# Performance work log

Measured on AMD Instinct MI355X. Metric: run time of the kernel, lower is better.

## Reference

```python
import jax, jax.numpy as jnp
import numpy as np

NUM_CLASSES = 10
BASE_TEMPERATURE = 0.07
TEMP = 0.1


def setup_inputs() -> dict:
    key = jax.random.key(0)
    k1, k2 = jax.random.split(key)
    features = jax.random.normal(k1, (8192, 128), dtype=jnp.float32)
    targets = jax.random.randint(k2, (8192,), 0, NUM_CLASSES, dtype=jnp.int64)
    return {"features": features, "targets": targets}


def reference(features, targets):
    bs = features.shape[0]
    dtype = features.dtype
    # one-hot label matrix -> positive mask via label agreement
    one_hot = jax.nn.one_hot(targets, NUM_CLASSES, dtype=dtype)          # [bs, C]
    mask_pos_full = one_hot @ one_hot.T                                  # [bs, bs], 1 if same class
    mask_negatives = jnp.ones((bs, bs), dtype=dtype) - mask_pos_full
    mask_positives = mask_pos_full - jnp.eye(bs, dtype=dtype)            # exclude self
    logits_mask = mask_positives + mask_negatives                        # == 1 - eye
    # pairwise similarity logits
    logits = (features @ features.T) / TEMP                              # [bs, bs]
    logits_max = jax.lax.stop_gradient(jnp.max(logits, axis=1, keepdims=True))
    logits = logits - logits_max
    exp_logits = jnp.exp(logits) * logits_mask
    log_prob = logits - jnp.log(jnp.sum(exp_logits, axis=1, keepdims=True) + 1e-20)
    mean_log_prob_pos = jnp.sum(mask_positives * log_prob, axis=1) / (
        jnp.sum(mask_positives, axis=1) + 1e-20
    )
    loss = -(TEMP / BASE_TEMPERATURE) * jnp.mean(mean_log_prob_pos)
    avg_pos = jnp.mean(jnp.sum(mask_positives, axis=1))
    avg_neg = jnp.mean(jnp.sum(mask_negatives, axis=1))
    return (loss, avg_pos, avg_neg)
```

## Files before the change

### kernel.cpp

```cpp
#include <hip/hip_runtime.h>

#define N 8192
#define KD 128
#define NCLS 10
#define NCH 8
#define CHUNK (N / NCH)

typedef __attribute__((ext_vector_type(4))) float floatx4;


__global__ __launch_bounds__(256) void k_conv(const float* __restrict__ F,
                                              const int* __restrict__ tgt,
                                              float* __restrict__ diag10,
                                              int* __restrict__ A10,
                                              int* __restrict__ B1,
                                              float* __restrict__ S,
                                              int* __restrict__ cnt,
                                              float* __restrict__ PS) {
    int t = threadIdx.x;
    if (blockIdx.x < 512) {
        int row0 = blockIdx.x * 16;
        if (t < 16) PS[row0 + t] = 0.f;
        int col4 = t & 31;
        int rg = t >> 5;
#pragma unroll
        for (int sw = 0; sw < 2; ++sw) {
            int row = row0 + sw * 8 + rg;
            float4 v = *(const float4*)(F + (size_t)row * KD + col4 * 4);
            float sq = v.x * v.x + v.y * v.y + v.z * v.z + v.w * v.w;
#pragma unroll
            for (int off = 16; off >= 1; off >>= 1) sq += __shfl_xor(sq, off);
            if (col4 == 0) diag10[row] = 10.f * sq;
            int da = __builtin_amdgcn_cvt_pk_fp8_f32(10.f * v.x, 10.f * v.y, 0, false);
            da = __builtin_amdgcn_cvt_pk_fp8_f32(10.f * v.z, 10.f * v.w, da, true);
            int db = __builtin_amdgcn_cvt_pk_fp8_f32(v.x, v.y, 0, false);
            db = __builtin_amdgcn_cvt_pk_fp8_f32(v.z, v.w, db, true);
            int rt = row >> 4, rl = row & 15;
            int ks = col4 >> 3, quad = (col4 & 7) >> 1, half = col4 & 1;
            int idx = rt * 512 + ks * 128 + quad * 32 + rl * 2 + half;
            A10[idx] = da;
            B1[idx] = db;
        }
    } else {
        int b = blockIdx.x - 512;
        int row0 = b * 128;
        int k = t & 127, h = t >> 7;
        __shared__ int lh[NCLS];
        if (t < NCLS) lh[t] = 0;
        __syncthreads();
        if (t < 128) atomicAdd(&lh[tgt[row0 + t]], 1);
        float local[NCLS];
#pragma unroll
        for (int c = 0; c < NCLS; ++c) local[c] = 0.f;
        for (int ii = 0; ii < 64; ++ii) {
            int row = row0 + h * 64 + ii;
            float v = F[(size_t)row * KD + k];
            int c = tgt[row];
#pragma unroll
            for (int cc = 0; cc < NCLS; ++cc) local[cc] += (cc == c) ? v : 0.f;
        }
        __shared__ float red[2][NCLS][KD];
#pragma unroll
        for (int cc = 0; cc < NCLS; ++cc) red[h][cc][k] = local[cc];
        __syncthreads();
        if (h == 0) {
#pragma unroll
            for (int cc = 0; cc < NCLS; ++cc)
                atomicAdd(&S[cc * KD + k], red[0][cc][k] + red[1][cc][k]);
            if (t < NCLS) atomicAdd(&cnt[t], lh[t]);
        }
    }
}

__global__ __launch_bounds__(256, 3) void k_pair(const unsigned char* __restrict__ Af,
                                                 const unsigned char* __restrict__ Bf,
                                                 const float* __restrict__ diag10,
                                                 float* __restrict__ PS) {
    int bx = blockIdx.x, ch = blockIdx.y;
    int tid = threadIdx.x;
    int w = tid >> 6, lane = tid & 63;
    int quad = lane >> 4, l16 = lane & 15;
    int row0 = bx * 64;

    float d = diag10[row0 + lane];
#pragma unroll
    for (int off = 32; off >= 1; off >>= 1) d = fminf(d, __shfl_xor(d, off));
    float thr = d - 60.f;

    long af[4][4];
#pragma unroll
    for (int it = 0; it < 4; ++it)
#pragma unroll
        for (int ks = 0; ks < 4; ++ks)
            af[it][ks] = *(const long*)(Af + (size_t)(bx * 4 + it) * 2048 + ks * 512 + lane * 8);

#pragma unroll
    for (int jj = 0; jj < 4; ++jj) {
        int col0 = ch * CHUNK + (jj * 4 + w) * 64;
        const unsigned char* bp = Bf + (size_t)(col0 >> 4) * 2048 + lane * 8;

        long bfr[4][4];
#pragma unroll
        for (int tj = 0; tj < 4; ++tj)
#pragma unroll
            for (int ks = 0; ks < 4; ++ks)
                bfr[tj][ks] = *(const long*)(bp + tj * 2048 + ks * 512);

        floatx4 acc[4][4];
#pragma unroll
        for (int it = 0; it < 4; ++it)
#pragma unroll
            for (int tj = 0; tj < 4; ++tj)
                acc[it][tj] = (floatx4){0.f, 0.f, 0.f, 0.f};

#pragma unroll
        for (int ks = 0; ks < 4; ++ks)
#pragma unroll
            for (int it = 0; it < 4; ++it)
#pragma unroll
                for (int tj = 0; tj < 4; ++tj)
                    acc[it][tj] = __builtin_amdgcn_mfma_f32_16x16x32_fp8_fp8(
                        af[it][ks], bfr[tj][ks], acc[it][tj], 0, 0, 0);

        float mx = -1e30f;
#pragma unroll
        for (int it = 0; it < 4; ++it)
#pragma unroll
            for (int tj = 0; tj < 4; ++tj) {
                float a01 = fmaxf(acc[it][tj][0], acc[it][tj][1]);
                float a23 = fmaxf(acc[it][tj][2], acc[it][tj][3]);
                mx = fmaxf(mx, fmaxf(a01, a23));
            }

        if (__any(mx > thr)) {
#pragma unroll
            for (int it = 0; it < 4; ++it)
#pragma unroll
                for (int r = 0; r < 4; ++r) {
                    int grow = row0 + it * 16 + quad * 4 + r;
                    float Mrow = diag10[grow];
                    float rs = 0.f;
#pragma unroll
                    for (int tj = 0; tj < 4; ++tj) {
                        int gcol = col0 + tj * 16 + l16;
                        float ev = __expf(acc[it][tj][r] - Mrow);
                        rs += (grow == gcol) ? 0.f : ev;
                    }
                    rs += __shfl_xor(rs, 1, 16);
                    rs += __shfl_xor(rs, 2, 16);
                    rs += __shfl_xor(rs, 4, 16);
                    rs += __shfl_xor(rs, 8, 16);
                    if (l16 == 0) atomicAdd(&PS[grow], rs);
                }
        }
    }
}

__global__ __launch_bounds__(256) void k_final(const float* __restrict__ F,
                                               const int* __restrict__ tgt,
                                               const float* __restrict__ diag10,
                                               const float* __restrict__ PS,
                                               const float* __restrict__ S,
                                               int* __restrict__ cnt,
                                               float* __restrict__ acc,
                                               float* __restrict__ out) {
    __shared__ float Ss[NCLS * KD];
    __shared__ int cs[NCLS];
    int t = threadIdx.x;
    for (int i = t; i < NCLS * KD; i += 256) Ss[i] = S[i];
    if (t < NCLS) cs[t] = cnt[t];
    __syncthreads();

    int g = t >> 2, q = t & 3;
    int row = blockIdx.x * 64 + g;
    int c = tgt[row];
    float dot = 0.f;
#pragma unroll
    for (int i = 0; i < 8; ++i) {
        float4 f = *(const float4*)(F + (size_t)row * KD + i * 16 + q * 4);
        float4 s = *(const float4*)(Ss + c * KD + i * 16 + q * 4);
        dot += f.x * s.x + f.y * s.y + f.z * s.z + f.w * s.w;
    }
    dot += __shfl_xor(dot, 1, 4);
    dot += __shfl_xor(dot, 2, 4);

    float mlp = 0.f;
    if (q == 0) {
        float M = diag10[row];
        float pp = 10.f * dot - M;
        float T = PS[row];
        float np = (float)(cs[c] - 1);
        mlp = (np < 0.5f) ? 0.f : (pp - np * (M + __logf(T + 1e-20f))) / np;
    }
#pragma unroll
    for (int off = 32; off >= 1; off >>= 1) mlp += __shfl_xor(mlp, off);
    __shared__ float wsum[4];
    int lane = t & 63, w = t >> 6;
    if (lane == 0) wsum[w] = mlp;
    __syncthreads();
    if (t == 0) {
        atomicAdd(acc, (wsum[0] + wsum[1]) + (wsum[2] + wsum[3]));
        __threadfence();
        int old = atomicAdd(&cnt[12], 1);
        if (old == (int)gridDim.x - 1) {
            float tot = atomicAdd(acc, 0.0f);
            double sp = 0.0, sn = 0.0;
            for (int cc = 0; cc < NCLS; ++cc) {
                double n = (double)cs[cc];
                sp += n * (n - 1.0);
                sn += n * ((double)N - n);
            }
            out[0] = (float)(-(0.1 / 0.07) * ((double)tot / (double)N));
            out[1] = (float)(sp / (double)N);
            out[2] = (float)(sn / (double)N);
        }
    }
}

extern "C" void kernel_launch(void* const* d_in, const int* in_sizes, int n_in,
                              void* d_out, int out_size, void* d_ws, size_t ws_size,
                              hipStream_t stream) {
    const float* F = (const float*)d_in[0];
    const int* tgt = (const int*)d_in[1];
    float* out = (float*)d_out;
    char* ws = (char*)d_ws;

    int* cnt = (int*)(ws);
    float* acc = (float*)(ws + 64);
    float* S = (float*)(ws + 128);
    float* PS = (float*)(ws + 8192);
    float* diag10 = (float*)(ws + 65536);
    int* A10 = (int*)(ws + (1u << 20));
    int* B1 = (int*)(ws + (2u << 20));

    hipMemsetAsync(ws, 0, 8192, stream);
    k_conv<<<576, 256, 0, stream>>>(F, tgt, diag10, A10, B1, S, cnt, PS);
    k_pair<<<dim3(N / 64, NCH), 256, 0, stream>>>((const unsigned char*)A10,
                                                  (const unsigned char*)B1, diag10, PS);
    k_final<<<N / 64, 256, 0, stream>>>(F, tgt, diag10, PS, S, cnt, acc, out);
}
```

Before: 98.07 us.

## Fuse class-sum reduction into conversion blocks and double pair-kernel column chunks

Each of the 512 conversion blocks now accumulates per-class feature sums and the label histogram in shared memory with LDS atomics, then flushes nonzero entries to global with atomics. This removes the separate 64 reduction blocks that each reread 128 rows. The pair kernel's column split goes from 8 to 16 chunks with half the inner iterations per block, giving more blocks for occupancy in exchange for reloading the A fragments more often. Global atomic traffic on S rises, since every block can touch up to 1280 entries.

```diff
diff --git a/kernel.cpp b/kernel.cpp
--- a/kernel.cpp
+++ b/kernel.cpp
@@ -3,7 +3,7 @@
 #define N 8192
 #define KD 128
 #define NCLS 10
-#define NCH 8
+#define NCH 16
 #define CHUNK (N / NCH)
 
 typedef __attribute__((ext_vector_type(4))) float floatx4;
@@ -17,59 +17,49 @@
                                               float* __restrict__ S,
                                               int* __restrict__ cnt,
                                               float* __restrict__ PS) {
+    __shared__ float red[NCLS][KD];
+    __shared__ int hist[NCLS];
     int t = threadIdx.x;
-    if (blockIdx.x < 512) {
-        int row0 = blockIdx.x * 16;
-        if (t < 16) PS[row0 + t] = 0.f;
-        int col4 = t & 31;
-        int rg = t >> 5;
-#pragma unroll
-        for (int sw = 0; sw < 2; ++sw) {
-            int row = row0 + sw * 8 + rg;
-            float4 v = *(const float4*)(F + (size_t)row * KD + col4 * 4);
-            float sq = v.x * v.x + v.y * v.y + v.z * v.z + v.w * v.w;
-#pragma unroll
-            for (int off = 16; off >= 1; off >>= 1) sq += __shfl_xor(sq, off);
-            if (col4 == 0) diag10[row] = 10.f * sq;
-            int da = __builtin_amdgcn_cvt_pk_fp8_f32(10.f * v.x, 10.f * v.y, 0, false);
-            da = __builtin_amdgcn_cvt_pk_fp8_f32(10.f * v.z, 10.f * v.w, da, true);
-            int db = __builtin_amdgcn_cvt_pk_fp8_f32(v.x, v.y, 0, false);
-            db = __builtin_amdgcn_cvt_pk_fp8_f32(v.z, v.w, db, true);
-            int rt = row >> 4, rl = row & 15;
-            int ks = col4 >> 3, quad = (col4 & 7) >> 1, half = col4 & 1;
-            int idx = rt * 512 + ks * 128 + quad * 32 + rl * 2 + half;
-            A10[idx] = da;
-            B1[idx] = db;
-        }
-    } else {
-        int b = blockIdx.x - 512;
-        int row0 = b * 128;
-        int k = t & 127, h = t >> 7;
-        __shared__ int lh[NCLS];
-        if (t < NCLS) lh[t] = 0;
-        __syncthreads();
-        if (t < 128) atomicAdd(&lh[tgt[row0 + t]], 1);
-        float local[NCLS];
-#pragma unroll
-        for (int c = 0; c < NCLS; ++c) local[c] = 0.f;
-        for (int ii = 0; ii < 64; ++ii) {
-            int row = row0 + h * 64 + ii;
-            float v = F[(size_t)row * KD + k];
-            int c = tgt[row];
-#pragma unroll
-            for (int cc = 0; cc < NCLS; ++cc) local[cc] += (cc == c) ? v : 0.f;
-        }
-        __shared__ float red[2][NCLS][KD];
-#pragma unroll
-        for (int cc = 0; cc < NCLS; ++cc) red[h][cc][k] = local[cc];
-        __syncthreads();
-        if (h == 0) {
-#pragma unroll
-            for (int cc = 0; cc < NCLS; ++cc)
-                atomicAdd(&S[cc * KD + k], red[0][cc][k] + red[1][cc][k]);
-            if (t < NCLS) atomicAdd(&cnt[t], lh[t]);
-        }
-    }
+    int row0 = blockIdx.x * 16;
+    if (t < NCLS) hist[t] = 0;
+    for (int i = t; i < NCLS * KD; i += 256) ((float*)red)[i] = 0.f;
+    __syncthreads();
+    if (t < 16) {
+        atomicAdd(&hist[tgt[row0 + t]], 1);
+        PS[row0 + t] = 0.f;
+    }
+
+    int col4 = t & 31;
+    int rg = t >> 5;
+#pragma unroll
+    for (int sw = 0; sw < 2; ++sw) {
+        int row = row0 + sw * 8 + rg;
+        float4 v = *(const float4*)(F + (size_t)row * KD + col4 * 4);
+        float sq = v.x * v.x + v.y * v.y + v.z * v.z + v.w * v.w;
+#pragma unroll
+        for (int off = 16; off >= 1; off >>= 1) sq += __shfl_xor(sq, off);
+        if (col4 == 0) diag10[row] = 10.f * sq;
+        int da = __builtin_amdgcn_cvt_pk_fp8_f32(10.f * v.x, 10.f * v.y, 0, false);
+        da = __builtin_amdgcn_cvt_pk_fp8_f32(10.f * v.z, 10.f * v.w, da, true);
+        int db = __builtin_amdgcn_cvt_pk_fp8_f32(v.x, v.y, 0, false);
+        db = __builtin_amdgcn_cvt_pk_fp8_f32(v.z, v.w, db, true);
+        int rt = row >> 4, rl = row & 15;
+        int ks = col4 >> 3, quad = (col4 & 7) >> 1, half = col4 & 1;
+        int idx = rt * 512 + ks * 128 + quad * 32 + rl * 2 + half;
+        A10[idx] = da;
+        B1[idx] = db;
+        int c = tgt[row];
+        atomicAdd(&red[c][col4 * 4 + 0], v.x);
+        atomicAdd(&red[c][col4 * 4 + 1], v.y);
+        atomicAdd(&red[c][col4 * 4 + 2], v.z);
+        atomicAdd(&red[c][col4 * 4 + 3], v.w);
+    }
+    __syncthreads();
+    for (int i = t; i < NCLS * KD; i += 256) {
+        float v = ((const float*)red)[i];
+        if (v != 0.f) atomicAdd(&S[i], v);
+    }
+    if (t < NCLS) atomicAdd(&cnt[t], hist[t]);
 }
 
 __global__ __launch_bounds__(256, 3) void k_pair(const unsigned char* __restrict__ Af,
@@ -95,7 +85,7 @@
             af[it][ks] = *(const long*)(Af + (size_t)(bx * 4 + it) * 2048 + ks * 512 + lane * 8);
 
 #pragma unroll
-    for (int jj = 0; jj < 4; ++jj) {
+    for (int jj = 0; jj < 2; ++jj) {
         int col0 = ch * CHUNK + (jj * 4 + w) * 64;
         const unsigned char* bp = Bf + (size_t)(col0 >> 4) * 2048 + lane * 8;
 
@@ -234,7 +224,7 @@
     int* B1 = (int*)(ws + (2u << 20));
 
     hipMemsetAsync(ws, 0, 8192, stream);
-    k_conv<<<576, 256, 0, stream>>>(F, tgt, diag10, A10, B1, S, cnt, PS);
+    k_conv<<<N / 16, 256, 0, stream>>>(F, tgt, diag10, A10, B1, S, cnt, PS);
     k_pair<<<dim3(N / 64, NCH), 256, 0, stream>>>((const unsigned char*)A10,
                                                   (const unsigned char*)B1, diag10, PS);
     k_final<<<N / 64, 256, 0, stream>>>(F, tgt, diag10, PS, S, cnt, acc, out);
```

Result: slower. 103.4 us (+5.5%).

## Fuse final reduction into pair kernel via per-row-block completion tickets

Applied to the files above, without the earlier changes.

Removes the separate k_final launch by having the last of the NCH chunk blocks for each row block (found with an atomic ticket counter per row block) compute that row block's loss contribution and the global finalization. This targets the launch gap and tail of an extra kernel. In exchange every pair block now pays a threadfence and an atomic, PS is read through an atomic to see other blocks' writes, and S and the class counts are read straight from global memory instead of being staged in LDS. The workspace layout is shifted so the tickets sit in the zeroed region.

```diff
diff --git a/kernel.cpp b/kernel.cpp
--- a/kernel.cpp
+++ b/kernel.cpp
@@ -75,7 +75,14 @@
 __global__ __launch_bounds__(256, 3) void k_pair(const unsigned char* __restrict__ Af,
                                                  const unsigned char* __restrict__ Bf,
                                                  const float* __restrict__ diag10,
-                                                 float* __restrict__ PS) {
+                                                 float* __restrict__ PS,
+                                                 const float* __restrict__ F,
+                                                 const int* __restrict__ tgt,
+                                                 const float* __restrict__ S,
+                                                 int* __restrict__ cnt,
+                                                 int* __restrict__ tk,
+                                                 float* __restrict__ acc,
+                                                 float* __restrict__ out) {
     int bx = blockIdx.x, ch = blockIdx.y;
     int tid = threadIdx.x;
     int w = tid >> 6, lane = tid & 63;
@@ -106,12 +113,12 @@
             for (int ks = 0; ks < 4; ++ks)
                 bfr[tj][ks] = *(const long*)(bp + tj * 2048 + ks * 512);
 
-        floatx4 acc[4][4];
+        floatx4 acm[4][4];
 #pragma unroll
         for (int it = 0; it < 4; ++it)
 #pragma unroll
             for (int tj = 0; tj < 4; ++tj)
-                acc[it][tj] = (floatx4){0.f, 0.f, 0.f, 0.f};
+                acm[it][tj] = (floatx4){0.f, 0.f, 0.f, 0.f};
 
 #pragma unroll
         for (int ks = 0; ks < 4; ++ks)
@@ -119,16 +126,16 @@
             for (int it = 0; it < 4; ++it)
 #pragma unroll
                 for (int tj = 0; tj < 4; ++tj)
-                    acc[it][tj] = __builtin_amdgcn_mfma_f32_16x16x32_fp8_fp8(
-                        af[it][ks], bfr[tj][ks], acc[it][tj], 0, 0, 0);
+                    acm[it][tj] = __builtin_amdgcn_mfma_f32_16x16x32_fp8_fp8(
+                        af[it][ks], bfr[tj][ks], acm[it][tj], 0, 0, 0);
 
         float mx = -1e30f;
 #pragma unroll
         for (int it = 0; it < 4; ++it)
 #pragma unroll
             for (int tj = 0; tj < 4; ++tj) {
-                float a01 = fmaxf(acc[it][tj][0], acc[it][tj][1]);
-                float a23 = fmaxf(acc[it][tj][2], acc[it][tj][3]);
+                float a01 = fmaxf(acm[it][tj][0], acm[it][tj][1]);
+                float a23 = fmaxf(acm[it][tj][2], acm[it][tj][3]);
                 mx = fmaxf(mx, fmaxf(a01, a23));
             }
 
@@ -143,7 +150,7 @@
 #pragma unroll
                     for (int tj = 0; tj < 4; ++tj) {
                         int gcol = col0 + tj * 16 + l16;
-                        float ev = __expf(acc[it][tj][r] - Mrow);
+                        float ev = __expf(acm[it][tj][r] - Mrow);
                         rs += (grow == gcol) ? 0.f : ev;
                     }
                     rs += __shfl_xor(rs, 1, 16);
@@ -154,31 +161,22 @@
                 }
         }
     }
-}
-
-__global__ __launch_bounds__(256) void k_final(const float* __restrict__ F,
-                                               const int* __restrict__ tgt,
-                                               const float* __restrict__ diag10,
-                                               const float* __restrict__ PS,
-                                               const float* __restrict__ S,
-                                               int* __restrict__ cnt,
-                                               float* __restrict__ acc,
-                                               float* __restrict__ out) {
-    __shared__ float Ss[NCLS * KD];
-    __shared__ int cs[NCLS];
-    int t = threadIdx.x;
-    for (int i = t; i < NCLS * KD; i += 256) Ss[i] = S[i];
-    if (t < NCLS) cs[t] = cnt[t];
+
+    __shared__ int winner;
+    __threadfence();
+    if (tid == 0) winner = (atomicAdd(&tk[bx], 1) == NCH - 1) ? 1 : 0;
     __syncthreads();
-
-    int g = t >> 2, q = t & 3;
-    int row = blockIdx.x * 64 + g;
+    if (!winner) return;
+    __threadfence();
+
+    int g = tid >> 2, q = tid & 3;
+    int row = row0 + g;
     int c = tgt[row];
     float dot = 0.f;
 #pragma unroll
     for (int i = 0; i < 8; ++i) {
         float4 f = *(const float4*)(F + (size_t)row * KD + i * 16 + q * 4);
-        float4 s = *(const float4*)(Ss + c * KD + i * 16 + q * 4);
+        float4 s = *(const float4*)(S + c * KD + i * 16 + q * 4);
         dot += f.x * s.x + f.y * s.y + f.z * s.z + f.w * s.w;
     }
     dot += __shfl_xor(dot, 1, 4);
@@ -188,25 +186,24 @@
     if (q == 0) {
         float M = diag10[row];
         float pp = 10.f * dot - M;
-        float T = PS[row];
-        float np = (float)(cs[c] - 1);
+        float T = atomicAdd(&PS[row], 0.f);
+        float np = (float)(cnt[c] - 1);
         mlp = (np < 0.5f) ? 0.f : (pp - np * (M + __logf(T + 1e-20f))) / np;
     }
 #pragma unroll
     for (int off = 32; off >= 1; off >>= 1) mlp += __shfl_xor(mlp, off);
     __shared__ float wsum[4];
-    int lane = t & 63, w = t >> 6;
     if (lane == 0) wsum[w] = mlp;
     __syncthreads();
-    if (t == 0) {
+    if (tid == 0) {
         atomicAdd(acc, (wsum[0] + wsum[1]) + (wsum[2] + wsum[3]));
         __threadfence();
         int old = atomicAdd(&cnt[12], 1);
-        if (old == (int)gridDim.x - 1) {
+        if (old == N / 64 - 1) {
             float tot = atomicAdd(acc, 0.0f);
             double sp = 0.0, sn = 0.0;
             for (int cc = 0; cc < NCLS; ++cc) {
-                double n = (double)cs[cc];
+                double n = (double)cnt[cc];
                 sp += n * (n - 1.0);
                 sn += n * ((double)N - n);
             }
@@ -227,7 +224,8 @@
 
     int* cnt = (int*)(ws);
     float* acc = (float*)(ws + 64);
-    float* S = (float*)(ws + 128);
+    int* tk = (int*)(ws + 128);
+    float* S = (float*)(ws + 1024);
     float* PS = (float*)(ws + 8192);
     float* diag10 = (float*)(ws + 65536);
     int* A10 = (int*)(ws + (1u << 20));
@@ -236,6 +234,6 @@
     hipMemsetAsync(ws, 0, 8192, stream);
     k_conv<<<576, 256, 0, stream>>>(F, tgt, diag10, A10, B1, S, cnt, PS);
     k_pair<<<dim3(N / 64, NCH), 256, 0, stream>>>((const unsigned char*)A10,
-                                                  (const unsigned char*)B1, diag10, PS);
-    k_final<<<N / 64, 256, 0, stream>>>(F, tgt, diag10, PS, S, cnt, acc, out);
+                                                  (const unsigned char*)B1, diag10, PS,
+                                                  F, tgt, S, cnt, tk, acc, out);
 }
```

New measurement: 167.8 us. 71.1% more time.
